# Optimization experiments

Hardware: AMD Instinct MI355X
Metric: run time of the kernel (lower is better)

The kernel has to match this reference:

```python
import jax, jax.numpy as jnp
import numpy as np

E = 8          # num_experts
K = 2          # top-k
H = 768        # hidden_size
F = 4 * H      # FFN intermediate (expansion_factor=4)
B, S = 2, 2048


def setup_inputs() -> dict:
    key = jax.random.key(0)
    ks = jax.random.split(key, 5)
    scale = 0.02
    return {
        "x": jax.random.normal(ks[0], (B, S, H), dtype=jnp.float32),
        "router_w": jax.random.normal(ks[1], (H, E), dtype=jnp.float32) * scale,
        "router_b": jnp.zeros((E,), dtype=jnp.float32),
        "w1": jax.random.normal(ks[2], (E, H, F), dtype=jnp.float32) * scale,
        "b1": jnp.zeros((E, F), dtype=jnp.float32),
        "w2": jax.random.normal(ks[3], (E, F, H), dtype=jnp.float32) * scale,
        "b2": jnp.zeros((E, H), dtype=jnp.float32),
    }


def reference(x, router_w, router_b, w1, b1, w2, b2):
    b, s, h = x.shape
    # Router
    scores = jnp.einsum("bsh,he->bse", x, router_w) + router_b
    probs = jax.nn.softmax(scores, axis=-1)                      # [b,s,E]
    top_probs, expert_ids = jax.lax.top_k(probs, K)              # [b,s,K]

    # Load-balance auxiliary loss (Switch-style)
    avg_probs = probs.mean(axis=(0, 1))                          # [E]
    top1 = jnp.argmax(probs, axis=-1).reshape(-1)                # [b*s]
    counts = jnp.zeros((E,), dtype=probs.dtype).at[top1].add(1.0)
    expert_freqs = counts / (b * s)
    bal_loss = 0.001 * jnp.dot(expert_freqs, avg_probs)

    # Normalize top-k gate weights
    norm_probs = top_probs / (top_probs.sum(axis=-1, keepdims=True) + 1e-9)  # [b,s,K]

    # Expert FFNs with ReLU^2 activation, computed per-expert (dense, then masked)
    h1 = jnp.einsum("bsh,ehf->ebsf", x, w1) + b1[:, None, None, :]
    h1 = jnp.square(jax.nn.relu(h1))
    h2 = jnp.einsum("ebsf,efh->ebsh", h1, w2) + b2[:, None, None, :]  # [E,b,s,H]

    # Combine: weight for expert e at token (b,s) = sum_k norm_probs * 1[ids_k == e]
    onehot = jax.nn.one_hot(expert_ids, E, dtype=x.dtype)        # [b,s,K,E]
    gate = jnp.einsum("bsk,bske->ebs", norm_probs, onehot)       # [E,b,s]
    out = jnp.einsum("ebs,ebsh->bsh", gate, h2)                  # [b,s,H]
    return out, bal_loss
```

## Files before the change

### kernel.cpp

```cpp
#include <hip/hip_runtime.h>
#include <hip/hip_bf16.h>
#include <stdint.h>

#define E_EXP 8
#define TOK   4096
#define HD    768
#define FD    3072
#define BK    64
#define CAP   8320
#define NKP2  2

typedef __attribute__((ext_vector_type(8))) short bf16x8;
typedef __attribute__((ext_vector_type(4))) float f32x4;

__device__ __forceinline__ unsigned short f2bf(float f) {
  union { float f; unsigned u; } v; v.f = f;
  unsigned r = v.u + 0x7fffu + ((v.u >> 16) & 1u);
  return (unsigned short)(r >> 16);
}
__device__ __forceinline__ float bf2f(unsigned short u) {
  union { unsigned u; float f; } v; v.u = ((unsigned)u) << 16;
  return v.f;
}

__device__ __forceinline__ void gload_lds16(const void* g, void* l) {
  __builtin_amdgcn_global_load_lds(
      (const __attribute__((address_space(1))) unsigned int*)g,
      (__attribute__((address_space(3))) unsigned int*)l, 16, 0, 0);
}

__device__ __forceinline__ int xcd_swizzle(int orig, int nwg) {
  int xcd = orig & 7, base = orig >> 3;
  int q = nwg >> 3, r = nwg & 7;
  return (xcd < r ? xcd * (q + 1) : r * (q + 1) + (xcd - r) * q) + base;
}

__global__ __launch_bounds__(256) void router_kernel(
    const float* __restrict__ x, const float* __restrict__ rw,
    const float* __restrict__ rb, unsigned short* __restrict__ xb,
    float* __restrict__ probs, int* __restrict__ ids,
    float* __restrict__ gates)
{
  __shared__ float lrw[E_EXP * HD];
  for (int i = threadIdx.x; i < E_EXP * HD; i += 256) {
    int h = i >> 3, e = i & 7;
    lrw[e * HD + h] = rw[i];
  }
  __syncthreads();
  const int wave = threadIdx.x >> 6, lane = threadIdx.x & 63;
  const int t = blockIdx.x * 4 + wave;
  const float* xrow = x + (size_t)t * HD;
  float acc[8] = {0, 0, 0, 0, 0, 0, 0, 0};
#pragma unroll
  for (int i = 0; i < HD / 64; ++i) {
    int h = i * 64 + lane;
    float xv = xrow[h];
    xb[(size_t)t * HD + h] = f2bf(xv);
#pragma unroll
    for (int e = 0; e < 8; ++e) acc[e] += xv * lrw[e * HD + h];
  }
#pragma unroll
  for (int d = 1; d < 64; d <<= 1) {
#pragma unroll
    for (int e = 0; e < 8; ++e) acc[e] += __shfl_xor(acc[e], d);
  }
  if (lane == 0) {
    float p[8]; float m = -1e30f, sum = 0.f;
#pragma unroll
    for (int e = 0; e < 8; ++e) { p[e] = acc[e] + rb[e]; m = fmaxf(m, p[e]); }
#pragma unroll
    for (int e = 0; e < 8; ++e) { p[e] = __expf(p[e] - m); sum += p[e]; }
    float inv = 1.f / sum;
#pragma unroll
    for (int e = 0; e < 8; ++e) p[e] *= inv;
    int i1 = 0;
#pragma unroll
    for (int e = 1; e < 8; ++e) if (p[e] > p[i1]) i1 = e;
    int i2 = (i1 == 0) ? 1 : 0;
#pragma unroll
    for (int e = 0; e < 8; ++e) if (e != i1 && p[e] > p[i2]) i2 = e;
    ids[t * 2] = i1; ids[t * 2 + 1] = i2;
    float den = 1.f / (p[i1] + p[i2] + 1e-9f);
    gates[t * 2] = p[i1] * den; gates[t * 2 + 1] = p[i2] * den;
#pragma unroll
    for (int e = 0; e < 8; ++e) probs[t * 8 + e] = p[e];
  }
}

#define TT 64
#define T1_TILES (E_EXP * (FD / TT) * (HD / TT))
#define T2_TILES (E_EXP * (HD / TT) * (FD / TT))
__global__ __launch_bounds__(256) void transpose_kernel(
    const float* __restrict__ w1, unsigned short* __restrict__ w1t,
    const float* __restrict__ w2, unsigned short* __restrict__ w2t)
{
  __shared__ unsigned short tile[TT][TT + 4];
  int id = blockIdx.x;
  const float* W; unsigned short* Wt; int Kd, Nd;
  if (id < T1_TILES) {
    W = w1; Wt = w1t; Kd = HD; Nd = FD;
  } else {
    id -= T1_TILES; W = w2; Wt = w2t; Kd = FD; Nd = HD;
  }
  const int nx = Nd / TT, nk = Kd / TT;
  const int e = id / (nx * nk);
  const int rem = id % (nx * nk);
  const int n0 = (rem % nx) * TT, k0 = (rem / nx) * TT;

  const int r0 = threadIdx.x >> 4;
  const int c4 = threadIdx.x & 15;
#pragma unroll
  for (int i = 0; i < 4; ++i) {
    int kk = r0 + i * 16;
    float4 v = *(const float4*)&W[((size_t)e * Kd + k0 + kk) * Nd + n0 + c4 * 4];
    tile[c4 * 4 + 0][kk] = f2bf(v.x);
    tile[c4 * 4 + 1][kk] = f2bf(v.y);
    tile[c4 * 4 + 2][kk] = f2bf(v.z);
    tile[c4 * 4 + 3][kk] = f2bf(v.w);
  }
  __syncthreads();
  const int n = threadIdx.x >> 2, kc = threadIdx.x & 3;
  unsigned short* dst = w1t == Wt ? Wt : Wt;
  dst = Wt + ((size_t)e * Nd + n0 + n) * Kd + k0 + kc * 16;
  bf16x8 a = *(const bf16x8*)&tile[n][kc * 16];
  bf16x8 b = *(const bf16x8*)&tile[n][kc * 16 + 8];
  *(bf16x8*)&dst[0] = a;
  *(bf16x8*)&dst[8] = b;
}

__global__ __launch_bounds__(1024) void stats_scatter_kernel(
    const int* __restrict__ ids, const float* __restrict__ probs,
    const float* __restrict__ gates, int* __restrict__ meta,
    int* __restrict__ token_list, int* __restrict__ pos_list,
    float* __restrict__ loss_out)
{
  __shared__ int cnt[8], top1c[8], cur[8];
  __shared__ float wsum[16][8];
  const int tid = threadIdx.x;
  if (tid < 8) { cnt[tid] = 0; top1c[tid] = 0; cur[tid] = 0; }
  __syncthreads();
  float local[8] = {0, 0, 0, 0, 0, 0, 0, 0};
  for (int t = tid; t < TOK; t += 1024) {
    int e0 = ids[2 * t], e1 = ids[2 * t + 1];
    atomicAdd(&cnt[e0], 1); atomicAdd(&cnt[e1], 1); atomicAdd(&top1c[e0], 1);
    const float4* pr = (const float4*)&probs[(size_t)t * 8];
    float4 a = pr[0], b = pr[1];
    local[0] += a.x; local[1] += a.y; local[2] += a.z; local[3] += a.w;
    local[4] += b.x; local[5] += b.y; local[6] += b.z; local[7] += b.w;
  }
#pragma unroll
  for (int d = 1; d < 64; d <<= 1) {
#pragma unroll
    for (int e = 0; e < 8; ++e) local[e] += __shfl_xor(local[e], d);
  }
  const int wave = tid >> 6, lane = tid & 63;
  if (lane == 0) {
#pragma unroll
    for (int e = 0; e < 8; ++e) wsum[wave][e] = local[e];
  }
  __syncthreads();
  if (tid == 0) {
    int total = 0, nt1 = 0;
    for (int e = 0; e < 8; ++e) {
      int c = cnt[e];
      meta[e] = c;
      meta[16 + e] = total;
      int t1 = (c + 127) >> 7;
      for (int i = 0; i < t1; ++i) { meta[64 + nt1 * 2] = e; meta[64 + nt1 * 2 + 1] = total + i * 128; ++nt1; }
      total += c;
    }
    meta[32] = nt1;
    float loss = 0.f;
    for (int e = 0; e < 8; ++e) {
      float psum = 0.f;
      for (int w = 0; w < 16; ++w) psum += wsum[w][e];
      loss += ((float)top1c[e] / 4096.f) * (psum / 4096.f);
    }
    loss_out[0] = 0.001f * loss;
  }
  __syncthreads();
  for (int t = tid; t < TOK; t += 1024) {
    int e0 = ids[2 * t], e1 = ids[2 * t + 1];
    int s0 = atomicAdd(&cur[e0], 1);
    int s1 = atomicAdd(&cur[e1], 1);
    int p0 = meta[16 + e0] + s0;
    int p1 = meta[16 + e1] + s1;
    token_list[p0] = t; pos_list[2 * t] = p0;
    token_list[p1] = t; pos_list[2 * t + 1] = p1;
  }
}

template<int BM, int BN, int MODE, int NW, int NKP>
__global__ __launch_bounds__(NW * 64, 4) void moe_gemm(
    const unsigned short* __restrict__ A,
    const unsigned short* __restrict__ Bw,
    const float* __restrict__ bias,
    const int* __restrict__ token_list,
    const int* __restrict__ meta,
    unsigned short* __restrict__ Cout,
    const int Kdim, const int NN)
{
  const int NY = NN / BN;
  const int wgid = xcd_swizzle(blockIdx.x, gridDim.x);
  const int mt = wgid / (NY * NKP);
  const int slot = wgid - mt * (NY * NKP);
  const int ny = slot % NY;
  const int kp = slot / NY;
  const int nt_total = meta[32];
  if (mt >= nt_total) return;
  const int* tmap = meta + 64;
  const int e = tmap[mt * 2], arow0 = tmap[mt * 2 + 1];
  const int ne_end = meta[16 + e] + meta[e];
  const int n0 = ny * BN;
  const int KLEN = Kdim / NKP;
  const int kbeg = kp * KLEN;
  unsigned short* Cp = Cout + (size_t)kp * CAP * NN;

  __shared__ unsigned short lA[BM * BK];
  __shared__ unsigned short lB[BN * BK];

  const int tid = threadIdx.x;
  const int wave = tid >> 6, lane = tid & 63;
  constexpr int WC_N = NW / 2;
  const int wr = wave / WC_N, wc = wave % WC_N;
  constexpr int WROWS = BM / 2;
  constexpr int WCOLS = BN / WC_N;
  constexpr int FM = WROWS / 16, FN = WCOLS / 16;
  constexpr int NCA = (BM / 8) / NW;
  constexpr int NCB = (BN / 8) / NW;

  const int kswz = ((lane & 7) ^ ((lane >> 3) & 7)) * 8;

  size_t aSrc[NCA];
#pragma unroll
  for (int i = 0; i < NCA; ++i) {
    int c = wave + i * NW;
    int r = c * 8 + (lane >> 3);
    int grow = (MODE == 0) ? token_list[arow0 + r] : (arow0 + r);
    aSrc[i] = (size_t)grow * Kdim + kbeg + kswz;
  }
  size_t bSrc[NCB];
#pragma unroll
  for (int i = 0; i < NCB; ++i) {
    int c = wave + i * NW;
    int n = n0 + c * 8 + (lane >> 3);
    bSrc[i] = ((size_t)e * NN + n) * Kdim + kbeg + kswz;
  }

  f32x4 acc[FM][FN] = {};

  for (int k0 = 0; k0 < KLEN; k0 += BK) {
#pragma unroll
    for (int i = 0; i < NCA; ++i)
      gload_lds16(A + aSrc[i] + k0, &lA[(wave + i * NW) * 512]);
#pragma unroll
    for (int i = 0; i < NCB; ++i)
      gload_lds16(Bw + bSrc[i] + k0, &lB[(wave + i * NW) * 512]);
    __syncthreads();
#pragma unroll
    for (int kk = 0; kk < BK; kk += 32) {
      bf16x8 af[FM], bfr[FN];
      const int lc = (kk >> 3) + (lane >> 4);
#pragma unroll
      for (int m2 = 0; m2 < FM; ++m2) {
        int row = wr * WROWS + m2 * 16 + (lane & 15);
        af[m2] = *(const bf16x8*)&lA[row * BK + ((lc ^ (row & 7)) << 3)];
      }
#pragma unroll
      for (int n2 = 0; n2 < FN; ++n2) {
        int row = wc * WCOLS + n2 * 16 + (lane & 15);
        bfr[n2] = *(const bf16x8*)&lB[row * BK + ((lc ^ (row & 7)) << 3)];
      }
#pragma unroll
      for (int m2 = 0; m2 < FM; ++m2)
#pragma unroll
        for (int n2 = 0; n2 < FN; ++n2)
          acc[m2][n2] = __builtin_amdgcn_mfma_f32_16x16x32_bf16(
              af[m2], bfr[n2], acc[m2][n2], 0, 0, 0);
    }
    __syncthreads();
  }

  const float* be = bias + (size_t)e * NN;
#pragma unroll
  for (int m2 = 0; m2 < FM; ++m2) {
    const int lr = wr * WROWS + m2 * 16 + (lane >> 4) * 4;
#pragma unroll
    for (int n2 = 0; n2 < FN; ++n2) {
      const int col = n0 + wc * WCOLS + n2 * 16 + (lane & 15);
      const float bv = (kp == 0) ? be[col] : 0.f;
#pragma unroll
      for (int j = 0; j < 4; ++j) {
        const int arow = arow0 + lr + j;
        if (arow < ne_end) {
          float v = acc[m2][n2][j] + bv;
          if (MODE == 0) { v = fmaxf(v, 0.f); v = v * v; }
          Cp[(size_t)arow * NN + col] = f2bf(v);
        }
      }
    }
  }
}

__global__ __launch_bounds__(256) void combine_kernel(
    const unsigned short* __restrict__ h2, const int* __restrict__ pos_list,
    const float* __restrict__ gates, float* __restrict__ out)
{
  const int wave = threadIdx.x >> 6, lane = threadIdx.x & 63;
  const int t = blockIdx.x * 4 + wave;
  const int p0 = pos_list[2 * t], p1 = pos_list[2 * t + 1];
  const float g0 = gates[2 * t], g1 = gates[2 * t + 1];
  float* o = out + (size_t)t * HD;
#pragma unroll
  for (int i = 0; i < 3; ++i) {
    int h = i * 256 + lane * 4;
    float4 o4 = {0.f, 0.f, 0.f, 0.f};
#pragma unroll
    for (int kp = 0; kp < NKP2; ++kp) {
      const unsigned short* base = h2 + (size_t)kp * CAP * HD;
      ushort4 a = *(const ushort4*)&base[(size_t)p0 * HD + h];
      ushort4 b = *(const ushort4*)&base[(size_t)p1 * HD + h];
      o4.x += g0 * bf2f(a.x) + g1 * bf2f(b.x);
      o4.y += g0 * bf2f(a.y) + g1 * bf2f(b.y);
      o4.z += g0 * bf2f(a.z) + g1 * bf2f(b.z);
      o4.w += g0 * bf2f(a.w) + g1 * bf2f(b.w);
    }
    *(float4*)&o[h] = o4;
  }
}

extern "C" void kernel_launch(void* const* d_in, const int* in_sizes, int n_in,
                              void* d_out, int out_size, void* d_ws, size_t ws_size,
                              hipStream_t stream)
{
  (void)in_sizes; (void)n_in; (void)ws_size; (void)out_size;
  const float* x  = (const float*)d_in[0];
  const float* rw = (const float*)d_in[1];
  const float* rb = (const float*)d_in[2];
  const float* w1 = (const float*)d_in[3];
  const float* b1 = (const float*)d_in[4];
  const float* w2 = (const float*)d_in[5];
  const float* b2 = (const float*)d_in[6];
  float* out = (float*)d_out;

  char* ws = (char*)d_ws;
  size_t off = 0;
  auto alloc = [&](size_t bytes) {
    off = (off + 255) & ~(size_t)255;
    void* p = ws + off;
    off += bytes;
    return p;
  };
  unsigned short* xb  = (unsigned short*)alloc((size_t)TOK * HD * 2);
  unsigned short* w1t = (unsigned short*)alloc((size_t)E_EXP * FD * HD * 2);
  unsigned short* w2t = (unsigned short*)alloc((size_t)E_EXP * HD * FD * 2);
  unsigned short* h1  = (unsigned short*)alloc((size_t)CAP * FD * 2);
  unsigned short* h2  = (unsigned short*)alloc((size_t)NKP2 * CAP * HD * 2);
  int*   token_list = (int*)alloc(CAP * 4);
  int*   pos_list   = (int*)alloc((size_t)TOK * 2 * 4);
  int*   ids        = (int*)alloc((size_t)TOK * 2 * 4);
  float* gates      = (float*)alloc((size_t)TOK * 2 * 4);
  float* probs      = (float*)alloc((size_t)TOK * 8 * 4);
  int*   meta       = (int*)alloc(1024 * 4);
  char*  ctrl       = (char*)token_list;
  size_t ctrl_bytes = (ws + off) - ctrl;

  hipMemsetAsync(ctrl, 0, ctrl_bytes, stream);

  router_kernel<<<TOK / 4, 256, 0, stream>>>(x, rw, rb, xb, probs, ids, gates);
  transpose_kernel<<<T1_TILES + T2_TILES, 256, 0, stream>>>(w1, w1t, w2, w2t);
  stats_scatter_kernel<<<1, 1024, 0, stream>>>(ids, probs, gates, meta,
      token_list, pos_list, out + (size_t)TOK * HD);
  moe_gemm<128, 128, 0, 4, 1><<<71 * (FD / 128), 256, 0, stream>>>(
      xb, w1t, b1, token_list, meta, h1, HD, FD);
  moe_gemm<128, 128, 1, 4, NKP2><<<71 * (HD / 128) * NKP2, 256, 0, stream>>>(
      h1, w2t, b2, token_list, meta, h2, FD, HD);
  combine_kernel<<<TOK / 4, 256, 0, stream>>>(h2, pos_list, gates, out);
}
```

Measured before the change: 199.0 us.

## Use 256x128 tiles with triple-buffered LDS ring pipeline in MoE GEMMs

Replaces the single-buffered 128x128 MoE GEMM with a 512-thread kernel that computes 256x128 tiles and cycles through a three-slot LDS ring. Global-to-LDS loads for future k-steps are issued while the current slot is consumed, using explicit vmcnt waits and barriers instead of __syncthreads around every tile. The goal is to hide memory latency and raise reuse per loaded tile. In exchange, occupancy drops (launch bounds of 2), tokens are padded more per expert (capacity raised to 10496), and the loop assumes the K-tile count is a multiple of three.

```diff
diff --git a/kernel.cpp b/kernel.cpp
--- a/kernel.cpp
+++ b/kernel.cpp
@@ -7,7 +7,7 @@
 #define HD    768
 #define FD    3072
 #define BK    64
-#define CAP   8320
+#define CAPR  10496
 #define NKP2  2
 
 typedef __attribute__((ext_vector_type(8))) short bf16x8;
@@ -120,8 +120,7 @@
   }
   __syncthreads();
   const int n = threadIdx.x >> 2, kc = threadIdx.x & 3;
-  unsigned short* dst = w1t == Wt ? Wt : Wt;
-  dst = Wt + ((size_t)e * Nd + n0 + n) * Kd + k0 + kc * 16;
+  unsigned short* dst = Wt + ((size_t)e * Nd + n0 + n) * Kd + k0 + kc * 16;
   bf16x8 a = *(const bf16x8*)&tile[n][kc * 16];
   bf16x8 b = *(const bf16x8*)&tile[n][kc * 16 + 8];
   *(bf16x8*)&dst[0] = a;
@@ -130,9 +129,8 @@
 
 __global__ __launch_bounds__(1024) void stats_scatter_kernel(
     const int* __restrict__ ids, const float* __restrict__ probs,
-    const float* __restrict__ gates, int* __restrict__ meta,
-    int* __restrict__ token_list, int* __restrict__ pos_list,
-    float* __restrict__ loss_out)
+    int* __restrict__ meta, int* __restrict__ token_list,
+    int* __restrict__ pos_list, float* __restrict__ loss_out)
 {
   __shared__ int cnt[8], top1c[8], cur[8];
   __shared__ float wsum[16][8];
@@ -160,16 +158,16 @@
   }
   __syncthreads();
   if (tid == 0) {
-    int total = 0, nt1 = 0;
+    int total = 0, nt2 = 0;
     for (int e = 0; e < 8; ++e) {
       int c = cnt[e];
       meta[e] = c;
       meta[16 + e] = total;
-      int t1 = (c + 127) >> 7;
-      for (int i = 0; i < t1; ++i) { meta[64 + nt1 * 2] = e; meta[64 + nt1 * 2 + 1] = total + i * 128; ++nt1; }
+      int t2 = (c + 255) >> 8;
+      for (int i = 0; i < t2; ++i) { meta[256 + nt2 * 2] = e; meta[256 + nt2 * 2 + 1] = total + i * 256; ++nt2; }
       total += c;
     }
-    meta[32] = nt1;
+    meta[33] = nt2;
     float loss = 0.f;
     for (int e = 0; e < 8; ++e) {
       float psum = 0.f;
@@ -190,8 +188,8 @@
   }
 }
 
-template<int BM, int BN, int MODE, int NW, int NKP>
-__global__ __launch_bounds__(NW * 64, 4) void moe_gemm(
+template<int MODE, int NKP>
+__global__ __launch_bounds__(512, 2) void moe_gemm_ring(
     const unsigned short* __restrict__ A,
     const unsigned short* __restrict__ Bw,
     const float* __restrict__ bias,
@@ -200,100 +198,111 @@
     unsigned short* __restrict__ Cout,
     const int Kdim, const int NN)
 {
+  constexpr int BM = 256, BN = 128;
   const int NY = NN / BN;
   const int wgid = xcd_swizzle(blockIdx.x, gridDim.x);
   const int mt = wgid / (NY * NKP);
   const int slot = wgid - mt * (NY * NKP);
   const int ny = slot % NY;
   const int kp = slot / NY;
-  const int nt_total = meta[32];
+  const int nt_total = meta[33];
   if (mt >= nt_total) return;
-  const int* tmap = meta + 64;
+  const int* tmap = meta + 256;
   const int e = tmap[mt * 2], arow0 = tmap[mt * 2 + 1];
   const int ne_end = meta[16 + e] + meta[e];
   const int n0 = ny * BN;
   const int KLEN = Kdim / NKP;
   const int kbeg = kp * KLEN;
-  unsigned short* Cp = Cout + (size_t)kp * CAP * NN;
-
-  __shared__ unsigned short lA[BM * BK];
-  __shared__ unsigned short lB[BN * BK];
+  unsigned short* Cp = Cout + (size_t)kp * CAPR * NN;
+
+  __shared__ unsigned short lA[3][BM * BK];
+  __shared__ unsigned short lB[3][BN * BK];
 
   const int tid = threadIdx.x;
-  const int wave = tid >> 6, lane = tid & 63;
-  constexpr int WC_N = NW / 2;
-  const int wr = wave / WC_N, wc = wave % WC_N;
-  constexpr int WROWS = BM / 2;
-  constexpr int WCOLS = BN / WC_N;
-  constexpr int FM = WROWS / 16, FN = WCOLS / 16;
-  constexpr int NCA = (BM / 8) / NW;
-  constexpr int NCB = (BN / 8) / NW;
-
+  const int w = tid >> 6, lane = tid & 63;
+  const int wr = w >> 2, wc = w & 3;
   const int kswz = ((lane & 7) ^ ((lane >> 3) & 7)) * 8;
 
-  size_t aSrc[NCA];
-#pragma unroll
-  for (int i = 0; i < NCA; ++i) {
-    int c = wave + i * NW;
-    int r = c * 8 + (lane >> 3);
+  size_t aSrc[4];
+#pragma unroll
+  for (int i = 0; i < 4; ++i) {
+    int r = (i * 8 + w) * 8 + (lane >> 3);
     int grow = (MODE == 0) ? token_list[arow0 + r] : (arow0 + r);
     aSrc[i] = (size_t)grow * Kdim + kbeg + kswz;
   }
-  size_t bSrc[NCB];
-#pragma unroll
-  for (int i = 0; i < NCB; ++i) {
-    int c = wave + i * NW;
-    int n = n0 + c * 8 + (lane >> 3);
+  size_t bSrc[2];
+#pragma unroll
+  for (int i = 0; i < 2; ++i) {
+    int n = n0 + (i * 8 + w) * 8 + (lane >> 3);
     bSrc[i] = ((size_t)e * NN + n) * Kdim + kbeg + kswz;
   }
 
-  f32x4 acc[FM][FN] = {};
-
-  for (int k0 = 0; k0 < KLEN; k0 += BK) {
-#pragma unroll
-    for (int i = 0; i < NCA; ++i)
-      gload_lds16(A + aSrc[i] + k0, &lA[(wave + i * NW) * 512]);
-#pragma unroll
-    for (int i = 0; i < NCB; ++i)
-      gload_lds16(Bw + bSrc[i] + k0, &lB[(wave + i * NW) * 512]);
-    __syncthreads();
-#pragma unroll
-    for (int kk = 0; kk < BK; kk += 32) {
-      bf16x8 af[FM], bfr[FN];
-      const int lc = (kk >> 3) + (lane >> 4);
-#pragma unroll
-      for (int m2 = 0; m2 < FM; ++m2) {
-        int row = wr * WROWS + m2 * 16 + (lane & 15);
-        af[m2] = *(const bf16x8*)&lA[row * BK + ((lc ^ (row & 7)) << 3)];
+  const int NT = KLEN / BK;
+  auto STAGE = [&](int buf, int kt) {
+    int k0 = (kt < NT ? kt : NT - 1) * BK;
+#pragma unroll
+    for (int i = 0; i < 4; ++i)
+      gload_lds16(A + aSrc[i] + k0, &lA[buf][(i * 8 + w) * 512]);
+#pragma unroll
+    for (int i = 0; i < 2; ++i)
+      gload_lds16(Bw + bSrc[i] + k0, &lB[buf][(i * 8 + w) * 512]);
+  };
+
+  f32x4 acc[8][2] = {};
+  auto COMPUTE = [&](int buf) {
+#pragma unroll
+    for (int kc = 0; kc < 2; ++kc) {
+      bf16x8 af[8], bf[2];
+#pragma unroll
+      for (int m = 0; m < 8; ++m) {
+        int row = wr * 128 + m * 16 + (lane & 15);
+        int lc = kc * 4 + (lane >> 4);
+        af[m] = *(const bf16x8*)&lA[buf][row * BK + ((lc ^ (row & 7)) << 3)];
       }
 #pragma unroll
-      for (int n2 = 0; n2 < FN; ++n2) {
-        int row = wc * WCOLS + n2 * 16 + (lane & 15);
-        bfr[n2] = *(const bf16x8*)&lB[row * BK + ((lc ^ (row & 7)) << 3)];
+      for (int n = 0; n < 2; ++n) {
+        int row = wc * 32 + n * 16 + (lane & 15);
+        int lc = kc * 4 + (lane >> 4);
+        bf[n] = *(const bf16x8*)&lB[buf][row * BK + ((lc ^ (row & 7)) << 3)];
       }
 #pragma unroll
-      for (int m2 = 0; m2 < FM; ++m2)
-#pragma unroll
-        for (int n2 = 0; n2 < FN; ++n2)
-          acc[m2][n2] = __builtin_amdgcn_mfma_f32_16x16x32_bf16(
-              af[m2], bfr[n2], acc[m2][n2], 0, 0, 0);
-    }
-    __syncthreads();
+      for (int m = 0; m < 8; ++m)
+#pragma unroll
+        for (int n = 0; n < 2; ++n)
+          acc[m][n] = __builtin_amdgcn_mfma_f32_16x16x32_bf16(
+              af[m], bf[n], acc[m][n], 0, 0, 0);
+    }
+  };
+
+  STAGE(0, 0);
+  STAGE(1, 1);
+  asm volatile("s_waitcnt vmcnt(6)" ::: "memory");
+  asm volatile("s_barrier" ::: "memory");
+  for (int kt = 0; kt + 3 <= NT; kt += 3) {
+    STAGE(2, kt + 2); COMPUTE(0);
+    asm volatile("s_waitcnt vmcnt(6)" ::: "memory");
+    asm volatile("s_barrier" ::: "memory");
+    STAGE(0, kt + 3); COMPUTE(1);
+    asm volatile("s_waitcnt vmcnt(6)" ::: "memory");
+    asm volatile("s_barrier" ::: "memory");
+    STAGE(1, kt + 4); COMPUTE(2);
+    asm volatile("s_waitcnt vmcnt(6)" ::: "memory");
+    asm volatile("s_barrier" ::: "memory");
   }
 
   const float* be = bias + (size_t)e * NN;
 #pragma unroll
-  for (int m2 = 0; m2 < FM; ++m2) {
-    const int lr = wr * WROWS + m2 * 16 + (lane >> 4) * 4;
-#pragma unroll
-    for (int n2 = 0; n2 < FN; ++n2) {
-      const int col = n0 + wc * WCOLS + n2 * 16 + (lane & 15);
+  for (int m = 0; m < 8; ++m) {
+    const int lr = wr * 128 + m * 16 + (lane >> 4) * 4;
+#pragma unroll
+    for (int n = 0; n < 2; ++n) {
+      const int col = n0 + wc * 32 + n * 16 + (lane & 15);
       const float bv = (kp == 0) ? be[col] : 0.f;
 #pragma unroll
       for (int j = 0; j < 4; ++j) {
         const int arow = arow0 + lr + j;
         if (arow < ne_end) {
-          float v = acc[m2][n2][j] + bv;
+          float v = acc[m][n][j] + bv;
           if (MODE == 0) { v = fmaxf(v, 0.f); v = v * v; }
           Cp[(size_t)arow * NN + col] = f2bf(v);
         }
@@ -317,7 +326,7 @@
     float4 o4 = {0.f, 0.f, 0.f, 0.f};
 #pragma unroll
     for (int kp = 0; kp < NKP2; ++kp) {
-      const unsigned short* base = h2 + (size_t)kp * CAP * HD;
+      const unsigned short* base = h2 + (size_t)kp * CAPR * HD;
       ushort4 a = *(const ushort4*)&base[(size_t)p0 * HD + h];
       ushort4 b = *(const ushort4*)&base[(size_t)p1 * HD + h];
       o4.x += g0 * bf2f(a.x) + g1 * bf2f(b.x);
@@ -354,9 +363,9 @@
   unsigned short* xb  = (unsigned short*)alloc((size_t)TOK * HD * 2);
   unsigned short* w1t = (unsigned short*)alloc((size_t)E_EXP * FD * HD * 2);
   unsigned short* w2t = (unsigned short*)alloc((size_t)E_EXP * HD * FD * 2);
-  unsigned short* h1  = (unsigned short*)alloc((size_t)CAP * FD * 2);
-  unsigned short* h2  = (unsigned short*)alloc((size_t)NKP2 * CAP * HD * 2);
-  int*   token_list = (int*)alloc(CAP * 4);
+  unsigned short* h1  = (unsigned short*)alloc((size_t)CAPR * FD * 2);
+  unsigned short* h2  = (unsigned short*)alloc((size_t)NKP2 * CAPR * HD * 2);
+  int*   token_list = (int*)alloc(CAPR * 4);
   int*   pos_list   = (int*)alloc((size_t)TOK * 2 * 4);
   int*   ids        = (int*)alloc((size_t)TOK * 2 * 4);
   float* gates      = (float*)alloc((size_t)TOK * 2 * 4);
@@ -369,11 +378,11 @@
 
   router_kernel<<<TOK / 4, 256, 0, stream>>>(x, rw, rb, xb, probs, ids, gates);
   transpose_kernel<<<T1_TILES + T2_TILES, 256, 0, stream>>>(w1, w1t, w2, w2t);
-  stats_scatter_kernel<<<1, 1024, 0, stream>>>(ids, probs, gates, meta,
+  stats_scatter_kernel<<<1, 1024, 0, stream>>>(ids, probs, meta,
       token_list, pos_list, out + (size_t)TOK * HD);
-  moe_gemm<128, 128, 0, 4, 1><<<71 * (FD / 128), 256, 0, stream>>>(
+  moe_gemm_ring<0, 1><<<39 * (FD / 128), 512, 0, stream>>>(
       xb, w1t, b1, token_list, meta, h1, HD, FD);
-  moe_gemm<128, 128, 1, 4, NKP2><<<71 * (HD / 128) * NKP2, 256, 0, stream>>>(
+  moe_gemm_ring<1, NKP2><<<39 * (HD / 128) * NKP2, 512, 0, stream>>>(
       h1, w2t, b2, token_list, meta, h2, FD, HD);
   combine_kernel<<<TOK / 4, 256, 0, stream>>>(h2, pos_list, gates, out);
 }
```

Result: slower. 244.4 us (+22.8%).
